# Performance work log

Hardware: AMD Instinct MI355X
Metric: run time of the kernel (lower is better)

## Reference

```python
import jax, jax.numpy as jnp
import numpy as np

N, n, m, k = 100000, 32, 16, 32
MU = 100.0  # bubble kernel scale (init arg mu)


def setup_inputs() -> dict:
    key = jax.random.key(0)
    ks = jax.random.split(key, 7)
    x = jax.random.normal(ks[0], (N,), dtype=jnp.float32)
    # torch.nn.Linear(N, n): weight [n, N], bias [n]
    encoder_w = jax.random.normal(ks[1], (n, N), dtype=jnp.float32) / np.float32(np.sqrt(N))
    encoder_b = jnp.zeros((n,), dtype=jnp.float32)
    # decoder parameter [n, N]
    decoder = jax.random.normal(ks[2], (n, N), dtype=jnp.float32) / np.float32(np.sqrt(n))
    # torch.nn.Linear(n, n*m): weight [n*m, n], bias [n*m]
    bw_w = jax.random.normal(ks[3], (n * m, n), dtype=jnp.float32) / np.float32(np.sqrt(n))
    bw_b = jnp.zeros((n * m,), dtype=jnp.float32)
    neighbour_distance = jax.random.uniform(ks[4], (N, k), dtype=jnp.float32)
    neighbour_id = jax.random.randint(ks[5], (N, k), 0, N)
    clustering_labels = jax.random.randint(ks[6], (N,), 0, m)
    return {
        "x": x,
        "encoder_w": encoder_w,
        "encoder_b": encoder_b,
        "decoder": decoder,
        "bw_w": bw_w,
        "bw_b": bw_b,
        "neighbour_distance": neighbour_distance,
        "neighbour_id": neighbour_id,
        "clustering_labels": clustering_labels,
    }


def reference(x, encoder_w, encoder_b, decoder, bw_w, bw_b,
              neighbour_distance, neighbour_id, clustering_labels):
    # encode: [N] -> [n]
    encoded = x @ encoder_w.T + encoder_b
    # per-basis, per-cluster bandwidths: sigmoid(Linear)/60 -> [n, m] -> expand to [n, N]
    bandwidths = jax.nn.sigmoid(encoded @ bw_w.T + bw_b) / 60.0
    w = bandwidths.reshape(n, m)[:, clustering_labels]  # [n, N]
    # bubble window: relu(1 - d^2 / (w*mu)^2) -> [n, N, k]
    window = jax.nn.relu(1.0 - neighbour_distance[None, :, :] ** 2
                         / (w[:, :, None] * MU) ** 2)
    # normalization over axis 1 (the N axis), faithful to the source's dim=1
    window = window / jnp.sum(window, axis=1, keepdims=True)
    # gather decoder rows at neighbours, weight, reduce over k: [n, N]
    convolved_basis = jnp.sum(decoder[:, neighbour_id] * window, axis=-1)
    # [n] @ [n, N] -> [N]
    return encoded @ convolved_basis
```

## Files before the change

### kernel.cpp

```cpp
#include <hip/hip_runtime.h>
#include <hip/hip_fp16.h>

#define N_PTS 100000
#define MU_F  100.0f

typedef unsigned int uint;
typedef _Float16 h2 __attribute__((ext_vector_type(2)));
typedef float f2 __attribute__((ext_vector_type(2)));

#define E_SCALE 16384.0f
#define E_SCALE_INV (1.0f / 16384.0f)

static __device__ inline h2 h2pack(float a, float b) {
    return __builtin_bit_cast(h2, __builtin_amdgcn_cvt_pkrtz(a, b));
}
static __device__ inline float fdot2f(h2 a, h2 b, float c) {
    return __builtin_amdgcn_fdot2(a, b, c, false);
}
static __device__ inline h2 h2fma(h2 a, h2 b, h2 c) {
#if __has_builtin(__builtin_elementwise_fma)
    return __builtin_elementwise_fma(a, b, c);
#else
    return a * b + c;
#endif
}
static __device__ inline h2 h2max(h2 a, h2 b) {
#if __has_builtin(__builtin_elementwise_max)
    return __builtin_elementwise_max(a, b);
#else
    h2 r;
    r.x = a.x > b.x ? a.x : b.x;
    r.y = a.y > b.y ? a.y : b.y;
    return r;
#endif
}

#define ENC_BLKS 256
#define TR_BLKS  1563
#define S_BLKS   1024
#define S_PCH    98
#define NCOPY    8
#define NPAIRS   (N_PTS / 2)
#define M_BLKS   1024
#define M_CH     49


__global__ __launch_bounds__(256) void k_prep_tr(const float* __restrict__ x,
                                                 const float* __restrict__ encW,
                                                 const float* __restrict__ encB,
                                                 float* __restrict__ enc,
                                                 const float* __restrict__ dec,
                                                 __half* __restrict__ decT) {
    int b = blockIdx.x;
    if (b < ENC_BLKS) {
        int row = b & 31;
        int chunk = b >> 5;
        const int CH = N_PTS / 8;
        int base = chunk * CH;
        const float4* W4 = reinterpret_cast<const float4*>(encW + (size_t)row * N_PTS + base);
        const float4* x4 = reinterpret_cast<const float4*>(x + base);
        const int nv = CH / 4;
        float acc = 0.f;
        for (int idx = threadIdx.x; idx < nv; idx += 256) {
            float4 w = W4[idx];
            float4 xv = x4[idx];
            acc += w.x * xv.x + w.y * xv.y + w.z * xv.z + w.w * xv.w;
        }
        #pragma unroll
        for (int off = 32; off > 0; off >>= 1) acc += __shfl_down(acc, off);
        __shared__ float sred[4];
        int wid = threadIdx.x >> 6;
        if ((threadIdx.x & 63) == 0) sred[wid] = acc;
        __syncthreads();
        if (threadIdx.x == 0) {
            float s = sred[0] + sred[1] + sred[2] + sred[3];
            if (chunk == 0) s += encB[row];
            atomicAdd(enc + row, s);
        }
    } else {
        __shared__ float tile[32][65];
        int j0 = (b - ENC_BLKS) * 64;
        int col = threadIdx.x & 63;
        int r0 = threadIdx.x >> 6;
        #pragma unroll
        for (int it = 0; it < 8; ++it) {
            int row = it * 4 + r0;
            int j = j0 + col;
            float v = (j < N_PTS) ? dec[(size_t)row * N_PTS + j] : 0.f;
            tile[row][col] = v;
        }
        __syncthreads();
        #pragma unroll
        for (int it = 0; it < 4; ++it) {
            int idx = it * 256 + threadIdx.x;
            int j = idx >> 4;
            int p = idx & 15;
            int jj = j0 + j;
            if (jj < N_PTS) {
                __half2 h = __halves2half2(__float2half(tile[2 * p][j]),
                                           __float2half(tile[2 * p + 1][j]));
                *reinterpret_cast<__half2*>(decT + (size_t)jj * 32 + 2 * p) = h;
            }
        }
    }
}

__global__ __launch_bounds__(256) void k_tab(const float* __restrict__ enc_g,
                                             const float* __restrict__ bw_w,
                                             const float* __restrict__ bw_b,
                                             float* __restrict__ invFG,
                                             h2* __restrict__ invHLG) {
    __shared__ float encL[32];
    __shared__ float invF[512];
    if (threadIdx.x < 32) encL[threadIdx.x] = enc_g[threadIdx.x];
    __syncthreads();
    for (int r = threadIdx.x; r < 512; r += 256) {
        int i = r >> 4, c = r & 15;
        const float4* wr4 = reinterpret_cast<const float4*>(bw_w + (size_t)r * 32);
        float z = bw_b[r];
        #pragma unroll
        for (int p4 = 0; p4 < 8; ++p4) {
            float4 wv = wr4[p4];
            z = fmaf(encL[4 * p4 + 0], wv.x, z);
            z = fmaf(encL[4 * p4 + 1], wv.y, z);
            z = fmaf(encL[4 * p4 + 2], wv.z, z);
            z = fmaf(encL[4 * p4 + 3], wv.w, z);
        }
        float s = 1.f / (1.f + __expf(-z));
        float wmu = s * (MU_F / 60.0f);
        float iv = 1.f / (wmu * wmu);
        invF[c * 32 + i] = iv;
        invFG[c * 32 + i] = iv;
    }
    __syncthreads();
    {
        int t = threadIdx.x;
        int c = t >> 4, q = (t >> 2) & 3, tt = t & 3;
        int i0 = q * 8 + 2 * tt;
        invHLG[t] = h2pack(fminf(invF[c * 32 + i0], 6.0e4f),
                           fminf(invF[c * 32 + i0 + 1], 6.0e4f));
    }
}

__global__ __launch_bounds__(256, 8) void k_S(const float* __restrict__ invFG,
                                              const float* __restrict__ nd,
                                              const int* __restrict__ labels,
                                              float* __restrict__ S8) {
    __shared__ float invF[512];
    if (threadIdx.x < 128)
        reinterpret_cast<float4*>(invF)[threadIdx.x] =
            reinterpret_cast<const float4*>(invFG)[threadIdx.x];
    __syncthreads();

    int kk = threadIdx.x & 31;
    int ig = threadIdx.x >> 5;
    int start = blockIdx.x * S_PCH;
    int jend = min(start + S_PCH, N_PTS);

    float a0 = 0.f, a1 = 0.f, a2 = 0.f, a3 = 0.f;

    auto ld4 = [&](int jbase, float* d, int* cc) {
        #pragma unroll
        for (int u = 0; u < 4; ++u) {
            int j = jbase + u;
            int jc = min(j, N_PTS - 1);
            float dv = __builtin_nontemporal_load(&nd[(size_t)jc * 32 + kk]);
            cc[u] = labels[jc];
            d[u] = (j < jend) ? dv : 1.0e15f;
        }
    };
    float dA[4], dB[4], dC[4]; int cA[4], cB[4], cC[4];
    ld4(start, dA, cA);
    ld4(start + 4, dB, cB);
    for (int jj = start; jj < jend; jj += 4) {
        ld4(jj + 8, dC, cC);
        #pragma unroll
        for (int u = 0; u < 4; ++u) {
            float4 iv = *reinterpret_cast<const float4*>(&invF[cA[u] * 32 + ig * 4]);
            float d2 = dA[u] * dA[u];
            a0 += fmaxf(fmaf(d2, -iv.x, 1.f), 0.f);
            a1 += fmaxf(fmaf(d2, -iv.y, 1.f), 0.f);
            a2 += fmaxf(fmaf(d2, -iv.z, 1.f), 0.f);
            a3 += fmaxf(fmaf(d2, -iv.w, 1.f), 0.f);
        }
        #pragma unroll
        for (int u = 0; u < 4; ++u) {
            dA[u] = dB[u]; cA[u] = cB[u];
            dB[u] = dC[u]; cB[u] = cC[u];
        }
    }

    float* Sc = S8 + (size_t)(blockIdx.x & (NCOPY - 1)) * 1024;
    int cell = (ig * 4) * 32 + kk;
    atomicAdd(&Sc[cell], a0);
    atomicAdd(&Sc[cell + 32], a1);
    atomicAdd(&Sc[cell + 64], a2);
    atomicAdd(&Sc[cell + 96], a3);
}

__global__ __launch_bounds__(256, 4) void k_main(const h2* __restrict__ invHLG,
                                                 const float* __restrict__ enc_g,
                                                 const float* __restrict__ S8,
                                                 const float* __restrict__ nd,
                                                 const int* __restrict__ nid,
                                                 const int* __restrict__ labels,
                                                 const __half* __restrict__ decT,
                                                 float* __restrict__ out) {
    __shared__ h2 invHL[256];
    __shared__ float Sred[1024];
    if (threadIdx.x < 64)
        reinterpret_cast<uint4*>(invHL)[threadIdx.x] =
            reinterpret_cast<const uint4*>(invHLG)[threadIdx.x];
    for (int t = threadIdx.x; t < 1024; t += 256) {
        float s = 0.f;
        #pragma unroll
        for (int c = 0; c < NCOPY; ++c)
            s += S8[(size_t)c * 1024 + t];
        Sred[t] = s;
    }
    __syncthreads();

    int lane = threadIdx.x & 63;
    int R = lane >> 2;
    int q = lane & 3;

    h2 EhA[4], EhB[4];
    #pragma unroll
    for (int t = 0; t < 4; ++t) {
        int i0 = q * 8 + 2 * t;
        float e0 = enc_g[i0], e1 = enc_g[i0 + 1];
        float sA0 = Sred[i0 * 32 + R],      sA1 = Sred[(i0 + 1) * 32 + R];
        float sB0 = Sred[i0 * 32 + R + 16], sB1 = Sred[(i0 + 1) * 32 + R + 16];
        EhA[t] = h2pack(e0 / sA0 * E_SCALE, e1 / sA1 * E_SCALE);
        EhB[t] = h2pack(e0 / sB0 * E_SCALE, e1 / sB1 * E_SCALE);
    }
    const h2 zero2 = h2pack(0.f, 0.f);
    const h2 one2 = h2pack(1.f, 1.f);

    int w = threadIdx.x >> 6;
    int start = blockIdx.x * M_CH;
    int pend = min(start + M_CH, NPAIRS);
    const uint4* decQ = reinterpret_cast<const uint4*>(decT);

    auto load_ldd = [&](int jp0, int jp1, int* id, float* dd) {
        #pragma unroll
        for (int s = 0; s < 4; ++s) {
            size_t idx = (size_t)((s >> 1) ? jp1 : jp0) * 32 + (s & 1) * 16 + R;
            id[s] = __builtin_nontemporal_load(&nid[idx]);
            dd[s] = __builtin_nontemporal_load(&nd[idx]);
        }
    };
    auto load_ih = [&](int c0, int c1, h2* ih0, h2* ih1) {
        uint4 a = *reinterpret_cast<const uint4*>(&invHL[c0 * 16 + q * 4]);
        uint4 bq = *reinterpret_cast<const uint4*>(&invHL[c1 * 16 + q * 4]);
        ih0[0] = __builtin_bit_cast(h2, a.x);  ih0[1] = __builtin_bit_cast(h2, a.y);
        ih0[2] = __builtin_bit_cast(h2, a.z);  ih0[3] = __builtin_bit_cast(h2, a.w);
        ih1[0] = __builtin_bit_cast(h2, bq.x); ih1[1] = __builtin_bit_cast(h2, bq.y);
        ih1[2] = __builtin_bit_cast(h2, bq.z); ih1[3] = __builtin_bit_cast(h2, bq.w);
    };

    for (int p = start + w; p < pend; p += 8) {
        bool has2 = (p + 4) < pend;
        int p2 = has2 ? (p + 4) : p;
        int jA0 = 2 * p,  jA1 = jA0 + 1;
        int jB0 = 2 * p2, jB1 = jB0 + 1;

        int cA0 = labels[jA0], cA1 = labels[jA1];
        int cB0 = labels[jB0], cB1 = labels[jB1];
        int idA[4], idB[4]; float ddA[4], ddB[4];
        load_ldd(jA0, jA1, idA, ddA);
        load_ldd(jB0, jB1, idB, ddB);
        uint4 rA[4], rB[4];
        #pragma unroll
        for (int s = 0; s < 4; ++s) {
            rA[s] = decQ[(size_t)idA[s] * 4 + q];
            rB[s] = decQ[(size_t)idB[s] * 4 + q];
        }
        h2 ihA0[4], ihA1[4], ihB0[4], ihB1[4];
        load_ih(cA0, cA1, ihA0, ihA1);
        load_ih(cB0, cB1, ihB0, ihB1);

        h2 mdA0, mdA1, mdA2, mdA3, mdB0, mdB1, mdB2, mdB3;
        {
            float d0 = ddA[0] * ddA[0], d1 = ddA[1] * ddA[1];
            float d2 = ddA[2] * ddA[2], d3 = ddA[3] * ddA[3];
            mdA0 = h2pack(-d0, -d0); mdA1 = h2pack(-d1, -d1);
            mdA2 = h2pack(-d2, -d2); mdA3 = h2pack(-d3, -d3);
            float e0 = ddB[0] * ddB[0], e1 = ddB[1] * ddB[1];
            float e2 = ddB[2] * ddB[2], e3 = ddB[3] * ddB[3];
            mdB0 = h2pack(-e0, -e0); mdB1 = h2pack(-e1, -e1);
            mdB2 = h2pack(-e2, -e2); mdB3 = h2pack(-e3, -e3);
        }

        float a0 = 0.f, a1 = 0.f, a2 = 0.f, a3 = 0.f;
        float b0 = 0.f, b1 = 0.f, b2 = 0.f, b3 = 0.f;
        #pragma unroll
        for (int t = 0; t < 4; ++t) {
            uint wA0 = (t == 0) ? rA[0].x : (t == 1) ? rA[0].y : (t == 2) ? rA[0].z : rA[0].w;
            uint wA1 = (t == 0) ? rA[1].x : (t == 1) ? rA[1].y : (t == 2) ? rA[1].z : rA[1].w;
            uint wA2 = (t == 0) ? rA[2].x : (t == 1) ? rA[2].y : (t == 2) ? rA[2].z : rA[2].w;
            uint wA3 = (t == 0) ? rA[3].x : (t == 1) ? rA[3].y : (t == 2) ? rA[3].z : rA[3].w;
            uint wB0 = (t == 0) ? rB[0].x : (t == 1) ? rB[0].y : (t == 2) ? rB[0].z : rB[0].w;
            uint wB1 = (t == 0) ? rB[1].x : (t == 1) ? rB[1].y : (t == 2) ? rB[1].z : rB[1].w;
            uint wB2 = (t == 0) ? rB[2].x : (t == 1) ? rB[2].y : (t == 2) ? rB[2].z : rB[2].w;
            uint wB3 = (t == 0) ? rB[3].x : (t == 1) ? rB[3].y : (t == 2) ? rB[3].z : rB[3].w;
            {
                h2 wv = h2max(h2fma(mdA0, ihA0[t], one2), zero2);
                a0 = fdot2f(wv * EhA[t], __builtin_bit_cast(h2, wA0), a0);
            }
            {
                h2 wv = h2max(h2fma(mdA1, ihA0[t], one2), zero2);
                a1 = fdot2f(wv * EhB[t], __builtin_bit_cast(h2, wA1), a1);
            }
            {
                h2 wv = h2max(h2fma(mdA2, ihA1[t], one2), zero2);
                a2 = fdot2f(wv * EhA[t], __builtin_bit_cast(h2, wA2), a2);
            }
            {
                h2 wv = h2max(h2fma(mdA3, ihA1[t], one2), zero2);
                a3 = fdot2f(wv * EhB[t], __builtin_bit_cast(h2, wA3), a3);
            }
            {
                h2 wv = h2max(h2fma(mdB0, ihB0[t], one2), zero2);
                b0 = fdot2f(wv * EhA[t], __builtin_bit_cast(h2, wB0), b0);
            }
            {
                h2 wv = h2max(h2fma(mdB1, ihB0[t], one2), zero2);
                b1 = fdot2f(wv * EhB[t], __builtin_bit_cast(h2, wB1), b1);
            }
            {
                h2 wv = h2max(h2fma(mdB2, ihB1[t], one2), zero2);
                b2 = fdot2f(wv * EhA[t], __builtin_bit_cast(h2, wB2), b2);
            }
            {
                h2 wv = h2max(h2fma(mdB3, ihB1[t], one2), zero2);
                b3 = fdot2f(wv * EhB[t], __builtin_bit_cast(h2, wB3), b3);
            }
        }
        float u = a0 + a1;
        float v = a2 + a3;
        float u2 = b0 + b1;
        float v2 = b2 + b3;
        #pragma unroll
        for (int off = 32; off > 0; off >>= 1) {
            u += __shfl_xor(u, off);
            v += __shfl_xor(v, off);
            u2 += __shfl_xor(u2, off);
            v2 += __shfl_xor(v2, off);
        }
        if (lane == 0) {
            out[jA0] = u * E_SCALE_INV;
            if (has2) out[jB0] = u2 * E_SCALE_INV;
        }
        if (lane == 32) {
            out[jA1] = v * E_SCALE_INV;
            if (has2) out[jB1] = v2 * E_SCALE_INV;
        }
    }
}

extern "C" void kernel_launch(void* const* d_in, const int* in_sizes, int n_in,
                              void* d_out, int out_size, void* d_ws, size_t ws_size,
                              hipStream_t stream) {
    const float* x     = (const float*)d_in[0];
    const float* enc_w = (const float*)d_in[1];
    const float* enc_b = (const float*)d_in[2];
    const float* dec   = (const float*)d_in[3];
    const float* bw_w  = (const float*)d_in[4];
    const float* bw_b  = (const float*)d_in[5];
    const float* nd    = (const float*)d_in[6];
    const int*   nid   = (const int*)d_in[7];
    const int*   labels= (const int*)d_in[8];
    float* out = (float*)d_out;

    char* ws = (char*)d_ws;
    float* enc    = (float*)(ws + 0);
    float* S8     = (float*)(ws + 128);
    float* invFG  = (float*)(ws + 32896);
    h2*    invHLG = (h2*)(ws + 34944);
    __half* decT  = (__half*)(ws + 532480);

    (void)hipMemsetAsync(d_ws, 0, 32896, stream);
    k_prep_tr<<<dim3(ENC_BLKS + TR_BLKS), dim3(256), 0, stream>>>(
        x, enc_w, enc_b, enc, dec, decT);
    k_tab<<<dim3(1), dim3(256), 0, stream>>>(enc, bw_w, bw_b, invFG, invHLG);
    k_S<<<dim3(S_BLKS), dim3(256), 0, stream>>>(invFG, nd, labels, S8);
    k_main<<<dim3(M_BLKS), dim3(256), 0, stream>>>(invHLG, enc, S8, nd, nid,
                                                   labels, decT, out);
}
```

Before: 167.6 us.

## Fold bandwidth table into k_S and drop memset and k_tab launches

Removes the hipMemsetAsync and the single-block k_tab kernel. The encoder now writes per-chunk partial sums instead of using atomics, an extra block in k_prep_tr zeroes the S accumulators, and every k_S block recomputes the 512-entry bandwidth table from bw_w staged through shared memory, with block 0 also writing the fp16 table that k_main reads. This cuts two serialized launches and their gaps, but each of the 1024 k_S blocks now repeats the small matvec and its extra syncs.

Result: no change. 169.0 us (+0.9%).

```diff
diff --git a/kernel.cpp b/kernel.cpp
--- a/kernel.cpp
+++ b/kernel.cpp
@@ -37,6 +37,7 @@
 
 #define ENC_BLKS 256
 #define TR_BLKS  1563
+#define Z_BLKS   1
 #define S_BLKS   1024
 #define S_PCH    98
 #define NCOPY    8
@@ -48,9 +49,10 @@
 __global__ __launch_bounds__(256) void k_prep_tr(const float* __restrict__ x,
                                                  const float* __restrict__ encW,
                                                  const float* __restrict__ encB,
-                                                 float* __restrict__ enc,
+                                                 float* __restrict__ enc_part,
                                                  const float* __restrict__ dec,
-                                                 __half* __restrict__ decT) {
+                                                 __half* __restrict__ decT,
+                                                 float* __restrict__ S8) {
     int b = blockIdx.x;
     if (b < ENC_BLKS) {
         int row = b & 31;
@@ -75,9 +77,9 @@
         if (threadIdx.x == 0) {
             float s = sred[0] + sred[1] + sred[2] + sred[3];
             if (chunk == 0) s += encB[row];
-            atomicAdd(enc + row, s);
-        }
-    } else {
+            enc_part[b] = s;
+        }
+    } else if (b < ENC_BLKS + TR_BLKS) {
         __shared__ float tile[32][65];
         int j0 = (b - ENC_BLKS) * 64;
         int col = threadIdx.x & 63;
@@ -102,58 +104,65 @@
                 *reinterpret_cast<__half2*>(decT + (size_t)jj * 32 + 2 * p) = h;
             }
         }
-    }
-}
-
-__global__ __launch_bounds__(256) void k_tab(const float* __restrict__ enc_g,
-                                             const float* __restrict__ bw_w,
-                                             const float* __restrict__ bw_b,
-                                             float* __restrict__ invFG,
-                                             h2* __restrict__ invHLG) {
+    } else {
+        float4 z; z.x = z.y = z.z = z.w = 0.f;
+        float4* S4 = reinterpret_cast<float4*>(S8);
+        for (int t = threadIdx.x; t < 2048; t += 256) S4[t] = z;
+    }
+}
+
+__global__ __launch_bounds__(256, 8) void k_S(const float* __restrict__ enc_part,
+                                              const float* __restrict__ bw_w,
+                                              const float* __restrict__ bw_b,
+                                              const float* __restrict__ nd,
+                                              const int* __restrict__ labels,
+                                              float* __restrict__ S8,
+                                              h2* __restrict__ invHLG) {
     __shared__ float encL[32];
     __shared__ float invF[512];
-    if (threadIdx.x < 32) encL[threadIdx.x] = enc_g[threadIdx.x];
+    __shared__ float rowbuf[64][33];
+    int t = threadIdx.x;
+    if (t < 32) {
+        float s = 0.f;
+        #pragma unroll
+        for (int c = 0; c < 8; ++c) s += enc_part[c * 32 + t];
+        encL[t] = s;
+    }
     __syncthreads();
-    for (int r = threadIdx.x; r < 512; r += 256) {
-        int i = r >> 4, c = r & 15;
-        const float4* wr4 = reinterpret_cast<const float4*>(bw_w + (size_t)r * 32);
-        float z = bw_b[r];
-        #pragma unroll
-        for (int p4 = 0; p4 < 8; ++p4) {
-            float4 wv = wr4[p4];
-            z = fmaf(encL[4 * p4 + 0], wv.x, z);
-            z = fmaf(encL[4 * p4 + 1], wv.y, z);
-            z = fmaf(encL[4 * p4 + 2], wv.z, z);
-            z = fmaf(encL[4 * p4 + 3], wv.w, z);
-        }
-        float s = 1.f / (1.f + __expf(-z));
-        float wmu = s * (MU_F / 60.0f);
-        float iv = 1.f / (wmu * wmu);
-        invF[c * 32 + i] = iv;
-        invFG[c * 32 + i] = iv;
-    }
-    __syncthreads();
-    {
-        int t = threadIdx.x;
+
+    const float4* bw4 = reinterpret_cast<const float4*>(bw_w);
+    for (int ch = 0; ch < 8; ++ch) {
+        #pragma unroll
+        for (int u = 0; u < 2; ++u) {
+            int f = ch * 512 + 2 * t + u;
+            float4 v = bw4[f];
+            int r = (f >> 3) - ch * 64;
+            int c4 = (f & 7) * 4;
+            rowbuf[r][c4 + 0] = v.x; rowbuf[r][c4 + 1] = v.y;
+            rowbuf[r][c4 + 2] = v.z; rowbuf[r][c4 + 3] = v.w;
+        }
+        __syncthreads();
+        if (t < 64) {
+            int r = ch * 64 + t;
+            float z = bw_b[r];
+            #pragma unroll
+            for (int p = 0; p < 32; ++p) z = fmaf(encL[p], rowbuf[t][p], z);
+            float sg = 1.f / (1.f + __expf(-z));
+            float wmu = sg * (MU_F / 60.0f);
+            int i = r >> 4, c = r & 15;
+            invF[c * 32 + i] = 1.f / (wmu * wmu);
+        }
+        __syncthreads();
+    }
+    if (blockIdx.x == 0) {
         int c = t >> 4, q = (t >> 2) & 3, tt = t & 3;
         int i0 = q * 8 + 2 * tt;
         invHLG[t] = h2pack(fminf(invF[c * 32 + i0], 6.0e4f),
                            fminf(invF[c * 32 + i0 + 1], 6.0e4f));
     }
-}
-
-__global__ __launch_bounds__(256, 8) void k_S(const float* __restrict__ invFG,
-                                              const float* __restrict__ nd,
-                                              const int* __restrict__ labels,
-                                              float* __restrict__ S8) {
-    __shared__ float invF[512];
-    if (threadIdx.x < 128)
-        reinterpret_cast<float4*>(invF)[threadIdx.x] =
-            reinterpret_cast<const float4*>(invFG)[threadIdx.x];
-    __syncthreads();
-
-    int kk = threadIdx.x & 31;
-    int ig = threadIdx.x >> 5;
+
+    int kk = t & 31;
+    int ig = t >> 5;
     int start = blockIdx.x * S_PCH;
     int jend = min(start + S_PCH, N_PTS);
 
@@ -199,7 +208,7 @@
 }
 
 __global__ __launch_bounds__(256, 4) void k_main(const h2* __restrict__ invHLG,
-                                                 const float* __restrict__ enc_g,
+                                                 const float* __restrict__ enc_part,
                                                  const float* __restrict__ S8,
                                                  const float* __restrict__ nd,
                                                  const int* __restrict__ nid,
@@ -208,9 +217,16 @@
                                                  float* __restrict__ out) {
     __shared__ h2 invHL[256];
     __shared__ float Sred[1024];
+    __shared__ float encLm[32];
     if (threadIdx.x < 64)
         reinterpret_cast<uint4*>(invHL)[threadIdx.x] =
             reinterpret_cast<const uint4*>(invHLG)[threadIdx.x];
+    if (threadIdx.x < 32) {
+        float s = 0.f;
+        #pragma unroll
+        for (int c = 0; c < 8; ++c) s += enc_part[c * 32 + threadIdx.x];
+        encLm[threadIdx.x] = s;
+    }
     for (int t = threadIdx.x; t < 1024; t += 256) {
         float s = 0.f;
         #pragma unroll
@@ -228,7 +244,7 @@
     #pragma unroll
     for (int t = 0; t < 4; ++t) {
         int i0 = q * 8 + 2 * t;
-        float e0 = enc_g[i0], e1 = enc_g[i0 + 1];
+        float e0 = encLm[i0], e1 = encLm[i0 + 1];
         float sA0 = Sred[i0 * 32 + R],      sA1 = Sred[(i0 + 1) * 32 + R];
         float sB0 = Sred[i0 * 32 + R + 16], sB1 = Sred[(i0 + 1) * 32 + R + 16];
         EhA[t] = h2pack(e0 / sA0 * E_SCALE, e1 / sA1 * E_SCALE);
@@ -374,17 +390,15 @@
     float* out = (float*)d_out;
 
     char* ws = (char*)d_ws;
-    float* enc    = (float*)(ws + 0);
-    float* S8     = (float*)(ws + 128);
-    float* invFG  = (float*)(ws + 32896);
-    h2*    invHLG = (h2*)(ws + 34944);
-    __half* decT  = (__half*)(ws + 532480);
-
-    (void)hipMemsetAsync(d_ws, 0, 32896, stream);
-    k_prep_tr<<<dim3(ENC_BLKS + TR_BLKS), dim3(256), 0, stream>>>(
-        x, enc_w, enc_b, enc, dec, decT);
-    k_tab<<<dim3(1), dim3(256), 0, stream>>>(enc, bw_w, bw_b, invFG, invHLG);
-    k_S<<<dim3(S_BLKS), dim3(256), 0, stream>>>(invFG, nd, labels, S8);
-    k_main<<<dim3(M_BLKS), dim3(256), 0, stream>>>(invHLG, enc, S8, nd, nid,
-                                                   labels, decT, out);
-}
+    float* enc_part = (float*)(ws + 0);
+    float* S8       = (float*)(ws + 1024);
+    h2*    invHLG   = (h2*)(ws + 33792);
+    __half* decT    = (__half*)(ws + 532480);
+
+    k_prep_tr<<<dim3(ENC_BLKS + TR_BLKS + Z_BLKS), dim3(256), 0, stream>>>(
+        x, enc_w, enc_b, enc_part, dec, decT, S8);
+    k_S<<<dim3(S_BLKS), dim3(256), 0, stream>>>(
+        enc_part, bw_w, bw_b, nd, labels, S8, invHLG);
+    k_main<<<dim3(M_BLKS), dim3(256), 0, stream>>>(invHLG, enc_part, S8,
+                                                   nd, nid, labels, decT, out);
+}
```
